# Performance work log

Measured on AMD Instinct MI355X. Metric: run time of the kernel, lower is better.

Reference implementation:

```python
import jax, jax.numpy as jnp
import numpy as np

ALPHA = 2.0  # spikingjelly ATan default

@jax.custom_vjp
def atan_spike(x):
    # Heaviside forward
    return (x >= 0).astype(x.dtype)

def _atan_fwd(x):
    return atan_spike(x), x

def _atan_bwd(x, g):
    c = (jnp.pi / 2.0) * ALPHA
    return (g * (ALPHA / 2.0) / (1.0 + (c * x) ** 2),)

atan_spike.defvjp(_atan_fwd, _atan_bwd)

def setup_inputs() -> dict:
    key = jax.random.key(0)
    k1, k2 = jax.random.split(key)
    T, B, N = 32, 128, 16384
    x_seq = jax.random.normal(k1, (T, B, N), dtype=jnp.float32)
    beta_raw = jnp.asarray(2.0, dtype=jnp.float32)  # _beta param; beta = sigmoid(_beta)
    return {"x_seq": x_seq, "beta_raw": beta_raw}

def reference(x_seq, beta_raw):
    beta = jax.nn.sigmoid(beta_raw)
    one = jnp.asarray(1.0, x_seq.dtype)

    def step(v, x_t):
        v = beta * v + x_t
        s = atan_spike(v - one)
        # hard reset, detach_reset=True
        v = v * (one - jax.lax.stop_gradient(s))
        return v, s

    v0 = jnp.zeros_like(x_seq[0])
    _, s_seq = jax.lax.scan(step, v0, x_seq)
    return s_seq
```

## Files before the change

kernel.cpp:

```cpp
#include <hip/hip_runtime.h>


#define T_STEPS 32
#define CH 8

typedef float vfloat4 __attribute__((ext_vector_type(4)));

#define ISSUE(buf, tc)                                                        \
    _Pragma("unroll")                                                         \
    for (int k = 0; k < CH; ++k) {                                            \
        unsigned voff = base16 + (unsigned)((tc) + k) * stride16;             \
        asm volatile("global_load_dwordx4 %0, %1, %2"                        \
                     : "=v"(buf[k])                                           \
                     : "v"(voff), "s"(xp));                                   \
    }

#define WAIT8 asm volatile("s_waitcnt vmcnt(8)" ::: "memory")

#define FENCE(buf)                                                            \
    _Pragma("unroll")                                                         \
    for (int k = 0; k < CH; ++k) asm volatile("" : "+v"(buf[k]));

#define CONSUME(buf, tc)                                                      \
    _Pragma("unroll")                                                         \
    for (int k = 0; k < CH; ++k) {                                            \
        vfloat4 xt = buf[k];                                                  \
        vfloat4 s;                                                            \
        _Pragma("unroll")                                                     \
        for (int c = 0; c < 4; ++c) {                                         \
               \
            v[c] = __fadd_rn(__fmul_rn(beta, v[c]), xt[c]);                   \
                                \
            s[c] = (__fadd_rn(v[c], -1.0f) >= 0.0f) ? 1.0f : 0.0f;            \
                                      \
            v[c] *= (1.0f - s[c]);                                            \
        }                                                                     \
        out[i + ((tc) + k) * bn4] = s;                                        \
    }

__global__ __launch_bounds__(256, 4) void plif_fwd_kernel(
    const vfloat4* __restrict__ xp, const float* __restrict__ beta_raw,
    vfloat4* __restrict__ out, int bn4)
{
    int i = blockIdx.x * blockDim.x + threadIdx.x;
    if (i >= bn4) return;

    float beta = 1.0f / (1.0f + expf(-beta_raw[0]));
    asm volatile("" : "+v"(beta));

    unsigned base16   = (unsigned)i * 16u;
    unsigned stride16 = (unsigned)bn4 * 16u;

    vfloat4 v = (vfloat4)(0.0f, 0.0f, 0.0f, 0.0f);
    vfloat4 A[CH], B[CH];

    ISSUE(A, 0);
    ISSUE(B, 8);
    WAIT8; FENCE(A); CONSUME(A, 0);
    ISSUE(A, 16);
    WAIT8; FENCE(B); CONSUME(B, 8);
    ISSUE(B, 24);
    WAIT8; FENCE(A); CONSUME(A, 16);
    WAIT8; FENCE(B); CONSUME(B, 24);
}

extern "C" void kernel_launch(void* const* d_in, const int* in_sizes, int n_in,
                              void* d_out, int out_size, void* d_ws, size_t ws_size,
                              hipStream_t stream) {
    const float* x        = (const float*)d_in[0];
    const float* beta_raw = (const float*)d_in[1];
    float* out            = (float*)d_out;

    int total = in_sizes[0];
    int bn    = total / T_STEPS;
    int bn4   = bn / 4;

    dim3 block(256);
    dim3 grid((bn4 + block.x - 1) / block.x);
    plif_fwd_kernel<<<grid, block, 0, stream>>>(
        (const vfloat4*)x, beta_raw, (vfloat4*)out, bn4);
}
```

Before: 455.0 us.

## Pack spikes into bitmasks, defer stores, and use finer double-buffered loads

Shrinks the load chunk from 8 to 4 vectors and double-buffers eight rounds, so that loads are issued right after each scan chunk instead of interleaving with stores. Spike results are packed into per-lane 32-bit masks during the scan, and all 32 output vectors are written at the end with nontemporal stores. This separates the read and write phases and avoids polluting the cache with output. The cost is a burst of stores at the end with no load overlap, plus smaller load batches in flight per thread.

```diff
diff --git a/kernel.cpp b/kernel.cpp
--- a/kernel.cpp
+++ b/kernel.cpp
@@ -2,7 +2,7 @@
 
 
 #define T_STEPS 32
-#define CH 8
+#define CH 4
 
 typedef float vfloat4 __attribute__((ext_vector_type(4)));
 
@@ -10,37 +10,37 @@
     _Pragma("unroll")                                                         \
     for (int k = 0; k < CH; ++k) {                                            \
         unsigned voff = base16 + (unsigned)((tc) + k) * stride16;             \
-        asm volatile("global_load_dwordx4 %0, %1, %2"                        \
+        asm volatile("global_load_dwordx4 %0, %1, %2"                         \
                      : "=v"(buf[k])                                           \
                      : "v"(voff), "s"(xp));                                   \
     }
 
-#define WAIT8 asm volatile("s_waitcnt vmcnt(8)" ::: "memory")
+#define WAITN(n) asm volatile("s_waitcnt vmcnt(" #n ")" ::: "memory")
 
 #define FENCE(buf)                                                            \
     _Pragma("unroll")                                                         \
     for (int k = 0; k < CH; ++k) asm volatile("" : "+v"(buf[k]));
 
-#define CONSUME(buf, tc)                                                      \
+#define SCAN(buf, tc)                                                         \
     _Pragma("unroll")                                                         \
     for (int k = 0; k < CH; ++k) {                                            \
         vfloat4 xt = buf[k];                                                  \
-        vfloat4 s;                                                            \
         _Pragma("unroll")                                                     \
         for (int c = 0; c < 4; ++c) {                                         \
                \
             v[c] = __fadd_rn(__fmul_rn(beta, v[c]), xt[c]);                   \
                                 \
-            s[c] = (__fadd_rn(v[c], -1.0f) >= 0.0f) ? 1.0f : 0.0f;            \
-                                      \
-            v[c] *= (1.0f - s[c]);                                            \
+            float d  = __fadd_rn(v[c], -1.0f);                                \
+            float sf = (d >= 0.0f) ? 1.0f : 0.0f;                             \
+            sp[c] |= ((d >= 0.0f) ? 1u : 0u) << ((tc) + k);                   \
+                                     \
+            v[c] *= (1.0f - sf);                                              \
         }                                                                     \
-        out[i + ((tc) + k) * bn4] = s;                                        \
     }
 
 __global__ __launch_bounds__(256, 4) void plif_fwd_kernel(
     const vfloat4* __restrict__ xp, const float* __restrict__ beta_raw,
-    vfloat4* __restrict__ out, int bn4)
+    vfloat4* __restrict__ op, int bn4)
 {
     int i = blockIdx.x * blockDim.x + threadIdx.x;
     if (i >= bn4) return;
@@ -52,16 +52,28 @@
     unsigned stride16 = (unsigned)bn4 * 16u;
 
     vfloat4 v = (vfloat4)(0.0f, 0.0f, 0.0f, 0.0f);
+    unsigned sp[4] = {0u, 0u, 0u, 0u};
     vfloat4 A[CH], B[CH];
 
     ISSUE(A, 0);
-    ISSUE(B, 8);
-    WAIT8; FENCE(A); CONSUME(A, 0);
-    ISSUE(A, 16);
-    WAIT8; FENCE(B); CONSUME(B, 8);
-    ISSUE(B, 24);
-    WAIT8; FENCE(A); CONSUME(A, 16);
-    WAIT8; FENCE(B); CONSUME(B, 24);
+    ISSUE(B, 4);
+    WAITN(4); FENCE(A); SCAN(A,  0); ISSUE(A,  8);
+    WAITN(4); FENCE(B); SCAN(B,  4); ISSUE(B, 12);
+    WAITN(4); FENCE(A); SCAN(A,  8); ISSUE(A, 16);
+    WAITN(4); FENCE(B); SCAN(B, 12); ISSUE(B, 20);
+    WAITN(4); FENCE(A); SCAN(A, 16); ISSUE(A, 24);
+    WAITN(4); FENCE(B); SCAN(B, 20); ISSUE(B, 28);
+    WAITN(4); FENCE(A); SCAN(A, 24);
+    WAITN(0); FENCE(B); SCAN(B, 28);
+
+    _Pragma("unroll")
+    for (int t = 0; t < T_STEPS; ++t) {
+        vfloat4 s;
+        _Pragma("unroll")
+        for (int c = 0; c < 4; ++c)
+            s[c] = ((sp[c] >> t) & 1u) ? 1.0f : 0.0f;
+        __builtin_nontemporal_store(s, &op[(unsigned)i + (unsigned)t * (unsigned)bn4]);
+    }
 }
 
 extern "C" void kernel_launch(void* const* d_in, const int* in_sizes, int n_in,
```

After: 500.2 us. +10.0%, slower.

## Replace hand-pipelined inline-asm loads with plain unrolled loop and higher occupancy

Applied to the files above, without the earlier changes.

Removes the manual double-buffered inline-assembly global loads and explicit vmcnt waits, and uses a simple fully unrolled time loop with ordinary vector loads and stores. Load scheduling is left to the compiler. The launch bound's minimum blocks per multiprocessor rises from 4 to 8, which tightens the register budget so more waves can be resident to hide memory latency. The risk is that the compiler hoists all 32 loads and then spills, or interleaves loads with stores less well than the manual schedule.

```diff
diff --git a/kernel.cpp b/kernel.cpp
--- a/kernel.cpp
+++ b/kernel.cpp
@@ -2,66 +2,35 @@
 
 
 #define T_STEPS 32
-#define CH 8
 
 typedef float vfloat4 __attribute__((ext_vector_type(4)));
 
-#define ISSUE(buf, tc)                                                        \
-    _Pragma("unroll")                                                         \
-    for (int k = 0; k < CH; ++k) {                                            \
-        unsigned voff = base16 + (unsigned)((tc) + k) * stride16;             \
-        asm volatile("global_load_dwordx4 %0, %1, %2"                        \
-                     : "=v"(buf[k])                                           \
-                     : "v"(voff), "s"(xp));                                   \
-    }
-
-#define WAIT8 asm volatile("s_waitcnt vmcnt(8)" ::: "memory")
-
-#define FENCE(buf)                                                            \
-    _Pragma("unroll")                                                         \
-    for (int k = 0; k < CH; ++k) asm volatile("" : "+v"(buf[k]));
-
-#define CONSUME(buf, tc)                                                      \
-    _Pragma("unroll")                                                         \
-    for (int k = 0; k < CH; ++k) {                                            \
-        vfloat4 xt = buf[k];                                                  \
-        vfloat4 s;                                                            \
-        _Pragma("unroll")                                                     \
-        for (int c = 0; c < 4; ++c) {                                         \
-               \
-            v[c] = __fadd_rn(__fmul_rn(beta, v[c]), xt[c]);                   \
-                                \
-            s[c] = (__fadd_rn(v[c], -1.0f) >= 0.0f) ? 1.0f : 0.0f;            \
-                                      \
-            v[c] *= (1.0f - s[c]);                                            \
-        }                                                                     \
-        out[i + ((tc) + k) * bn4] = s;                                        \
-    }
-
-__global__ __launch_bounds__(256, 4) void plif_fwd_kernel(
+__global__ __launch_bounds__(256, 8) void plif_fwd_kernel(
     const vfloat4* __restrict__ xp, const float* __restrict__ beta_raw,
-    vfloat4* __restrict__ out, int bn4)
+    vfloat4* __restrict__ op, int bn4)
 {
     int i = blockIdx.x * blockDim.x + threadIdx.x;
     if (i >= bn4) return;
 
     float beta = 1.0f / (1.0f + expf(-beta_raw[0]));
-    asm volatile("" : "+v"(beta));
 
-    unsigned base16   = (unsigned)i * 16u;
-    unsigned stride16 = (unsigned)bn4 * 16u;
+    const vfloat4* rp = xp + i;
+    vfloat4*       wp = op + i;
 
     vfloat4 v = (vfloat4)(0.0f, 0.0f, 0.0f, 0.0f);
-    vfloat4 A[CH], B[CH];
 
-    ISSUE(A, 0);
-    ISSUE(B, 8);
-    WAIT8; FENCE(A); CONSUME(A, 0);
-    ISSUE(A, 16);
-    WAIT8; FENCE(B); CONSUME(B, 8);
-    ISSUE(B, 24);
-    WAIT8; FENCE(A); CONSUME(A, 16);
-    WAIT8; FENCE(B); CONSUME(B, 24);
+    #pragma unroll
+    for (int t = 0; t < T_STEPS; ++t) {
+        vfloat4 xt = rp[(size_t)t * (unsigned)bn4];
+        vfloat4 s;
+        #pragma unroll
+        for (int c = 0; c < 4; ++c) {
+            v[c] = __fadd_rn(__fmul_rn(beta, v[c]), xt[c]);
+            s[c] = (__fadd_rn(v[c], -1.0f) >= 0.0f) ? 1.0f : 0.0f;
+            v[c] *= (1.0f - s[c]);
+        }
+        wp[(size_t)t * (unsigned)bn4] = s;
+    }
 }
 
 extern "C" void kernel_launch(void* const* d_in, const int* in_sizes, int n_in,
```

Result: no change. 450.5 us (-1.0%).
